# Performance work log

Measured on AMD Instinct MI355X. Metric: run time of the kernel, lower is better.

## Reference

```python
import jax, jax.numpy as jnp
import numpy as np

MAX_DISP = 4                 # max_displacement
OUT_DIM = 2 * MAX_DISP + 1   # 9 -> 81 displacement channels


def setup_inputs() -> dict:
    key = jax.random.key(0)
    k1, k2 = jax.random.split(key)
    B, C, H, W = 8, 64, 192, 192
    x1 = jax.random.normal(k1, (B, C, H, W), dtype=jnp.float32)
    x2 = jax.random.normal(k2, (B, C, H, W), dtype=jnp.float32)
    return {"x1": x1, "x2": x2}


def reference(x1, x2):
    # x1, x2: [B, C, H, W]; stride1 = stride2 = 1 (default-equivalent config)
    B, C, H, W = x1.shape
    # pad x2 by max_displacement on each spatial side
    x2p = jnp.pad(x2, ((0, 0), (0, 0), (MAX_DISP, MAX_DISP), (MAX_DISP, MAX_DISP)))
    # for each displacement (i, j): channel-mean of x1 * shifted window of x2
    cv = [
        jnp.mean(x1 * jax.lax.dynamic_slice(x2p, (0, 0, i, j), (B, C, H, W)), axis=1)
        for i in range(OUT_DIM)
        for j in range(OUT_DIM)
    ]
    # torch.cat of keepdim means == stack along channel: [B, OUT_DIM**2, H, W]
    return jnp.stack(cv, axis=1)
```

## Files before the change

### kernel.cpp

```cpp
#include <hip/hip_runtime.h>


constexpr int MAXD = 4;
constexpr int OD   = 9;
constexpr int ND   = 81;
constexpr int TB_W = 32;
constexpr int TB_H = 8;
constexpr int CK   = 8;
constexpr int X2W  = 40;
constexpr int X2H  = 16;
constexpr int NT   = 576;

constexpr int Bc = 8, Cc = 64, Hc = 192, Wc = 192;
constexpr int HW = Hc * Wc;
constexpr int NCHUNK = Cc / CK;
constexpr int CSTEP  = CK * HW;
constexpr int TILE_F = CK * X2H * X2W;
constexpr int NF4    = TILE_F / 4;

__device__ __align__(16) float g_zero4[4];

__device__ inline void gload_lds16(const float* g, float* l) {
    __builtin_amdgcn_global_load_lds(
        (const __attribute__((address_space(1))) void*)g,
        (__attribute__((address_space(3))) void*)l, 16, 0, 0);
}

__global__ __launch_bounds__(NT, 4) void corr_kernel(
    const float* __restrict__ x1, const float* __restrict__ x2,
    float* __restrict__ out)
{
    __shared__ __align__(16) float s2[2][TILE_F];

    const int tid = threadIdx.x;
    const int g   = tid & 63;
    const int di  = tid >> 6;
    const int gw4 = (g & 7) * 4;
    const int gh  = g >> 3;

    const int w0 = blockIdx.x * TB_W;
    const int h0 = blockIdx.y * TB_H;
    const int b  = blockIdx.z;

    const float* x1b = x1 + (long)b * Cc * HW;
    const float* x2b = x2 + (long)b * Cc * HW;

    int  q0, q1, q2;
    bool st0, st1, st2;
    {
        auto slot = [&](int i, int& q, bool& st) {
            int idx = tid + i * NT;
            if (idx >= NF4) idx = 0;
            int c  = idx / (NF4 / CK);
            int r  = idx - c * (NF4 / CK);
            int y  = r / (X2W / 4);
            int x4 = r - y * (X2W / 4);
            int gy = h0 + y - MAXD;
            int gx = w0 + x4 * 4 - MAXD;
            st = ((unsigned)gy < (unsigned)Hc) && ((unsigned)gx < (unsigned)Wc);
            q  = c * HW + gy * Wc + gx;
        };
        slot(0, q0, st0);
        slot(1, q1, st1);
        slot(2, q2, st2);
    }

    float acc[OD][4];
#pragma unroll
    for (int dj = 0; dj < OD; ++dj)
#pragma unroll
        for (int p = 0; p < 4; ++p) acc[dj][p] = 0.f;

    int poff = (h0 + gh) * Wc + (w0 + gw4);
    const int roff = (gh + di) * X2W + gw4;

    auto stage = [&](int k, float* buf) {
        const int cb = k * CSTEP;
        float* d = buf + (unsigned)tid * 4;
        const float* z = g_zero4;
        gload_lds16(st0 ? x2b + cb + q0 : z, d);
        gload_lds16(st1 ? x2b + cb + q1 : z, d + NT * 4);
        if (tid < 2 * 64) {
            gload_lds16(st2 ? x2b + cb + q2 : z, d + 2 * NT * 4);
        }
    };

    stage(0, s2[0]);
    __syncthreads();

#pragma unroll 1
    for (int k = 0; k < NCHUNK; ++k) {
        float* bufA = s2[k & 1];
        float* bufB = s2[(k & 1) ^ 1];

        if (k + 1 < NCHUNK) stage(k + 1, bufB);

#pragma unroll
        for (int c = 0; c < CK; ++c) {
            float4 a = *(const float4*)(x1b + poff);
            poff += HW;
            const float* wr = bufA + c * (X2H * X2W) + roff;
            float4 b0 = *(const float4*)(wr);
            float4 b1 = *(const float4*)(wr + 4);
            float4 b2 = *(const float4*)(wr + 8);
            float win[12] = {b0.x, b0.y, b0.z, b0.w,
                             b1.x, b1.y, b1.z, b1.w,
                             b2.x, b2.y, b2.z, b2.w};
            float av[4] = {a.x, a.y, a.z, a.w};
#pragma unroll
            for (int dj = 0; dj < OD; ++dj)
#pragma unroll
                for (int p = 0; p < 4; ++p)
                    acc[dj][p] = fmaf(av[p], win[dj + p], acc[dj][p]);
        }

        __syncthreads();
    }

    const float scale = 1.0f / 64.0f;
    float* ob = out + (((long)b * ND + di * OD) * Hc + (h0 + gh)) * Wc + (w0 + gw4);
#pragma unroll
    for (int dj = 0; dj < OD; ++dj) {
        float4 v;
        v.x = acc[dj][0] * scale;
        v.y = acc[dj][1] * scale;
        v.z = acc[dj][2] * scale;
        v.w = acc[dj][3] * scale;
        *(float4*)(ob + (long)dj * HW) = v;
    }
}

extern "C" void kernel_launch(void* const* d_in, const int* in_sizes, int n_in,
                              void* d_out, int out_size, void* d_ws, size_t ws_size,
                              hipStream_t stream) {
    const float* x1 = (const float*)d_in[0];
    const float* x2 = (const float*)d_in[1];
    float* out = (float*)d_out;
    dim3 grid(Wc / TB_W, Hc / TB_H, Bc);
    corr_kernel<<<grid, NT, 0, stream>>>(x1, x2, out);
}
```

Before: 282.9 us.

## Split displacement rows across blocks and widen per-thread tile to 8 pixels

Each block now covers a 32x16 spatial tile and one of three groups of three displacement rows, using 192 threads (3 waves) instead of 576. Each thread computes 8 adjacent output pixels per displacement instead of 4, so every loaded x2 window value feeds more FMAs and LDS traffic per FMA drops. The channel chunk shrinks to 4, and a 1D grid with batch-fastest ordering is used to improve L2 sharing of x2 tiles. The trade-offs are that x1 is re-read three times across blocks, the accumulator count grows to 72 registers per thread, and the launch bound drops to 2 blocks per CU.

New measurement: 300.9 us. 6.4% more time.

```diff
diff --git a/kernel.cpp b/kernel.cpp
--- a/kernel.cpp
+++ b/kernel.cpp
@@ -5,18 +5,27 @@
 constexpr int OD   = 9;
 constexpr int ND   = 81;
 constexpr int TB_W = 32;
-constexpr int TB_H = 8;
-constexpr int CK   = 8;
-constexpr int X2W  = 40;
-constexpr int X2H  = 16;
-constexpr int NT   = 576;
+constexpr int TB_H = 16;
+constexpr int TWp  = 8;
+constexpr int CK   = 4;
+constexpr int NW   = 3;
+constexpr int NT   = NW * 64;
+constexpr int XROWS = TB_H + NW - 1;
+constexpr int XSTR  = 44;
 
 constexpr int Bc = 8, Cc = 64, Hc = 192, Wc = 192;
 constexpr int HW = Hc * Wc;
-constexpr int NCHUNK = Cc / CK;
-constexpr int CSTEP  = CK * HW;
-constexpr int TILE_F = CK * X2H * X2W;
-constexpr int NF4    = TILE_F / 4;
+constexpr int NCH   = Cc / CK;
+constexpr int CSTEP = CK * HW;
+constexpr int F4_PER_CH = XROWS * XSTR / 4;
+constexpr int SLAB_F4_REAL = CK * F4_PER_CH;
+constexpr int SLOTS = 5;
+constexpr int SLAB_F4 = SLOTS * NT;
+constexpr int SLAB_F  = SLAB_F4 * 4;
+
+constexpr int GX = Wc / TB_W;
+constexpr int GY = Hc / TB_H;
+constexpr int NBLK = GX * GY * Bc * 3;
 
 __device__ __align__(16) float g_zero4[4];
 
@@ -26,107 +35,112 @@
         (__attribute__((address_space(3))) void*)l, 16, 0, 0);
 }
 
-__global__ __launch_bounds__(NT, 4) void corr_kernel(
+__global__ __launch_bounds__(NT, 2) void corr_kernel(
     const float* __restrict__ x1, const float* __restrict__ x2,
     float* __restrict__ out)
 {
-    __shared__ __align__(16) float s2[2][TILE_F];
+    __shared__ __align__(16) float s2[2][SLAB_F];
 
-    const int tid = threadIdx.x;
-    const int g   = tid & 63;
-    const int di  = tid >> 6;
-    const int gw4 = (g & 7) * 4;
-    const int gh  = g >> 3;
+    const int tid  = threadIdx.x;
+    const int lane = tid & 63;
+    const int wid  = tid >> 6;
+    const int px8  = (lane & 3) * 8;
+    const int gh   = lane >> 2;
 
-    const int w0 = blockIdx.x * TB_W;
-    const int h0 = blockIdx.y * TB_H;
-    const int b  = blockIdx.z;
+    const int n    = blockIdx.x;
+    const int b    = n & 7;
+    const int t    = n >> 3;
+    const int g3   = t % 3;
+    const int tile = t / 3;
+    const int ty   = tile / GX;
+    const int tx   = tile - ty * GX;
+    const int w0   = tx * TB_W;
+    const int h0   = ty * TB_H;
+    const int di   = 3 * g3 + wid;
 
     const float* x1b = x1 + (long)b * Cc * HW;
     const float* x2b = x2 + (long)b * Cc * HW;
 
-    int  q0, q1, q2;
-    bool st0, st1, st2;
-    {
-        auto slot = [&](int i, int& q, bool& st) {
-            int idx = tid + i * NT;
-            if (idx >= NF4) idx = 0;
-            int c  = idx / (NF4 / CK);
-            int r  = idx - c * (NF4 / CK);
-            int y  = r / (X2W / 4);
-            int x4 = r - y * (X2W / 4);
-            int gy = h0 + y - MAXD;
-            int gx = w0 + x4 * 4 - MAXD;
-            st = ((unsigned)gy < (unsigned)Hc) && ((unsigned)gx < (unsigned)Wc);
-            q  = c * HW + gy * Wc + gx;
-        };
-        slot(0, q0, st0);
-        slot(1, q1, st1);
-        slot(2, q2, st2);
+    int  q[SLOTS];
+    int  d4[SLOTS];
+    bool ok[SLOTS];
+#pragma unroll
+    for (int i = 0; i < SLOTS; ++i) {
+        int s = wid * (SLOTS * 64) + i * 64 + lane;
+        d4[i] = s * 4;
+        int sr = (s < SLAB_F4_REAL) ? s : 0;
+        int c  = sr / F4_PER_CH;
+        int rm = sr - c * F4_PER_CH;
+        int r  = rm / (XSTR / 4);
+        int x4 = rm - r * (XSTR / 4);
+        int rg = h0 + 3 * g3 - MAXD + r;
+        int gc = w0 - MAXD + x4 * 4;
+        ok[i] = (s < SLAB_F4_REAL) && (x4 < 10) &&
+                ((unsigned)rg < (unsigned)Hc) && ((unsigned)gc < (unsigned)(Wc - 3));
+        q[i]  = c * HW + rg * Wc + gc;
     }
 
-    float acc[OD][4];
+    float acc[OD][TWp];
 #pragma unroll
     for (int dj = 0; dj < OD; ++dj)
 #pragma unroll
-        for (int p = 0; p < 4; ++p) acc[dj][p] = 0.f;
+        for (int p = 0; p < TWp; ++p) acc[dj][p] = 0.f;
 
-    int poff = (h0 + gh) * Wc + (w0 + gw4);
-    const int roff = (gh + di) * X2W + gw4;
+    int poff = (h0 + gh) * Wc + (w0 + px8);
+    const int ldr = gh + wid;
 
     auto stage = [&](int k, float* buf) {
         const int cb = k * CSTEP;
-        float* d = buf + (unsigned)tid * 4;
         const float* z = g_zero4;
-        gload_lds16(st0 ? x2b + cb + q0 : z, d);
-        gload_lds16(st1 ? x2b + cb + q1 : z, d + NT * 4);
-        if (tid < 2 * 64) {
-            gload_lds16(st2 ? x2b + cb + q2 : z, d + 2 * NT * 4);
-        }
+#pragma unroll
+        for (int i = 0; i < SLOTS; ++i)
+            gload_lds16(ok[i] ? x2b + cb + q[i] : z, buf + d4[i]);
     };
 
     stage(0, s2[0]);
     __syncthreads();
 
 #pragma unroll 1
-    for (int k = 0; k < NCHUNK; ++k) {
+    for (int k = 0; k < NCH; ++k) {
         float* bufA = s2[k & 1];
         float* bufB = s2[(k & 1) ^ 1];
 
-        if (k + 1 < NCHUNK) stage(k + 1, bufB);
+        if (k + 1 < NCH) stage(k + 1, bufB);
 
 #pragma unroll
         for (int c = 0; c < CK; ++c) {
-            float4 a = *(const float4*)(x1b + poff);
+            float4 a0 = *(const float4*)(x1b + poff);
+            float4 a1 = *(const float4*)(x1b + poff + 4);
             poff += HW;
-            const float* wr = bufA + c * (X2H * X2W) + roff;
+            const float* wr = bufA + c * (XROWS * XSTR) + ldr * XSTR + px8;
             float4 b0 = *(const float4*)(wr);
             float4 b1 = *(const float4*)(wr + 4);
             float4 b2 = *(const float4*)(wr + 8);
-            float win[12] = {b0.x, b0.y, b0.z, b0.w,
-                             b1.x, b1.y, b1.z, b1.w,
-                             b2.x, b2.y, b2.z, b2.w};
-            float av[4] = {a.x, a.y, a.z, a.w};
+            float4 b3 = *(const float4*)(wr + 12);
+            float win[16] = {b0.x, b0.y, b0.z, b0.w,  b1.x, b1.y, b1.z, b1.w,
+                             b2.x, b2.y, b2.z, b2.w,  b3.x, b3.y, b3.z, b3.w};
+            float av[8]  = {a0.x, a0.y, a0.z, a0.w,  a1.x, a1.y, a1.z, a1.w};
 #pragma unroll
             for (int dj = 0; dj < OD; ++dj)
 #pragma unroll
-                for (int p = 0; p < 4; ++p)
-                    acc[dj][p] = fmaf(av[p], win[dj + p], acc[dj][p]);
+                for (int p = 0; p < TWp; ++p)
+                    acc[dj][p] = fmaf(av[p], win[p + dj], acc[dj][p]);
         }
 
         __syncthreads();
     }
 
     const float scale = 1.0f / 64.0f;
-    float* ob = out + (((long)b * ND + di * OD) * Hc + (h0 + gh)) * Wc + (w0 + gw4);
+    float* ob = out + (((long)b * ND + di * OD) * Hc + (h0 + gh)) * Wc + (w0 + px8);
 #pragma unroll
     for (int dj = 0; dj < OD; ++dj) {
-        float4 v;
-        v.x = acc[dj][0] * scale;
-        v.y = acc[dj][1] * scale;
-        v.z = acc[dj][2] * scale;
-        v.w = acc[dj][3] * scale;
-        *(float4*)(ob + (long)dj * HW) = v;
+        float4 v0, v1;
+        v0.x = acc[dj][0] * scale;  v0.y = acc[dj][1] * scale;
+        v0.z = acc[dj][2] * scale;  v0.w = acc[dj][3] * scale;
+        v1.x = acc[dj][4] * scale;  v1.y = acc[dj][5] * scale;
+        v1.z = acc[dj][6] * scale;  v1.w = acc[dj][7] * scale;
+        *(float4*)(ob + (long)dj * HW)     = v0;
+        *(float4*)(ob + (long)dj * HW + 4) = v1;
     }
 }
 
@@ -136,6 +150,5 @@
     const float* x1 = (const float*)d_in[0];
     const float* x2 = (const float*)d_in[1];
     float* out = (float*)d_out;
-    dim3 grid(Wc / TB_W, Hc / TB_H, Bc);
-    corr_kernel<<<grid, NT, 0, stream>>>(x1, x2, out);
+    corr_kernel<<<dim3(NBLK), NT, 0, stream>>>(x1, x2, out);
 }
```
